# Optimization experiments

Hardware: AMD Instinct MI355X
Metric: run time of the kernel (lower is better)

Reference implementation:

```python
import jax, jax.numpy as jnp
import numpy as np

S, B, E, H, V, L = 128, 64, 512, 1024, 10000, 2


def setup_inputs() -> dict:
    key = jax.random.key(0)
    ks = jax.random.split(key, 10)
    s = 0.02  # weight scale ~ uniform(-k,k) magnitude
    return {
        "inputs": jax.random.randint(ks[0], (S, B), 0, V),
        "hidden": jnp.zeros((L, B, H), jnp.float32),
        "emb": jax.random.normal(ks[1], (V, E), jnp.float32) * 0.1,
        "Wx0": jax.random.normal(ks[2], (3, H, E), jnp.float32) * s,
        "Uh0": jax.random.normal(ks[3], (3, H, H), jnp.float32) * s,
        "b0": jax.random.normal(ks[4], (3, H), jnp.float32) * s,
        "Wx1": jax.random.normal(ks[5], (3, H, H), jnp.float32) * s,
        "Uh1": jax.random.normal(ks[6], (3, H, H), jnp.float32) * s,
        "b1": jax.random.normal(ks[7], (3, H), jnp.float32) * s,
        "Wd": jax.random.normal(ks[8], (V, H), jnp.float32) * 0.1,
        "bd": jnp.zeros((V,), jnp.float32),
    }


def _gru_cell(xp, h, U, b):
    # xp: (3,B,H) precomputed input projections in [r,z,h] order
    r = jax.nn.sigmoid(xp[0] + h @ U[0].T + b[0])
    z = jax.nn.sigmoid(xp[1] + h @ U[1].T + b[1])
    h_tilde = jnp.tanh(xp[2] + (r * h) @ U[2].T + b[2])
    return (1.0 - z) * h + z * h_tilde


def reference(inputs, hidden, emb, Wx0, Uh0, b0, Wx1, Uh1, b1, Wd, bd):
    x_embs = emb[inputs]                                   # [S,B,E]
    # precompute layer-0 input projections across all timesteps
    xa0 = jnp.einsum("sbe,goe->sgbo", x_embs, Wx0)        # [S,3,B,H]

    def step(carry, xa0_t):
        h0, h1 = carry
        h0n = _gru_cell(xa0_t, h0, Uh0, b0)
        xp1 = jnp.einsum("bk,gok->gbo", h0n, Wx1)          # [3,B,H]
        h1n = _gru_cell(xp1, h1, Uh1, b1)
        return (h0n, h1n), h1n

    (h0f, h1f), hs1 = jax.lax.scan(step, (hidden[0], hidden[1]), xa0)
    logits = jnp.einsum("sbh,vh->sbv", hs1, Wd) + bd       # [S,B,V]
    return logits, jnp.stack([h0f, h1f])
```

## Files before the change

kernel.cpp:

```cpp
#include <hip/hip_runtime.h>
#include <hip/hip_bf16.h>

#define SLEN 128
#define BAT 64
#define EDIM 512
#define HDIM 1024
#define VOC 10000
#define VPAD 10112
#define NWG_REC 192
#define TPB_REC 512

typedef short v8s __attribute__((ext_vector_type(8)));
typedef float v4f __attribute__((ext_vector_type(4)));
typedef unsigned short u16;

__device__ __forceinline__ u16 f2bf(float f) {
  unsigned u = __float_as_uint(f);
  u += 0x7fffu + ((u >> 16) & 1u);
  return (u16)(u >> 16);
}
__device__ __forceinline__ float bf2f(u16 b) {
  return __uint_as_float(((unsigned)b) << 16);
}
__device__ __forceinline__ float sigm(float x) { return 1.f / (1.f + __expf(-x)); }
__device__ __forceinline__ float tanh_f(float x) { return 1.f - 2.f / (1.f + __expf(2.f * x)); }

__device__ __forceinline__ void st_f32(float* p, float v) {
  __hip_atomic_store(p, v, __ATOMIC_RELAXED, __HIP_MEMORY_SCOPE_AGENT);
}
__device__ __forceinline__ float ld_f32(const float* p) {
  return __hip_atomic_load(p, __ATOMIC_RELAXED, __HIP_MEMORY_SCOPE_AGENT);
}
__device__ __forceinline__ float ld_bf16(const unsigned* base, int elem) {
  unsigned pr = __hip_atomic_load(base + (elem >> 1), __ATOMIC_RELAXED, __HIP_MEMORY_SCOPE_AGENT);
  return bf2f((u16)((elem & 1) ? (pr >> 16) : (pr & 0xffffu)));
}
__device__ __forceinline__ void st_bf16_pair(unsigned* base, int elem, u16 val, int l) {
  unsigned p = (unsigned)__shfl_xor((int)val, 1);
  if ((l & 1) == 0)
    __hip_atomic_store(base + (elem >> 1), (unsigned)val | (p << 16),
                       __ATOMIC_RELAXED, __HIP_MEMORY_SCOPE_AGENT);
}

__device__ __forceinline__ void gbar(int* bar, int ph, int wg, int t) {
  asm volatile("s_waitcnt vmcnt(0) lgkmcnt(0)" ::: "memory");
  __syncthreads();
  if (t == 0)
    __hip_atomic_store(&bar[wg], ph, __ATOMIC_RELAXED, __HIP_MEMORY_SCOPE_AGENT);
  if (t < 64) {
    for (;;) {
      int v0 = __hip_atomic_load(&bar[t],       __ATOMIC_RELAXED, __HIP_MEMORY_SCOPE_AGENT);
      int v1 = __hip_atomic_load(&bar[64 + t],  __ATOMIC_RELAXED, __HIP_MEMORY_SCOPE_AGENT);
      int v2 = __hip_atomic_load(&bar[128 + t], __ATOMIC_RELAXED, __HIP_MEMORY_SCOPE_AGENT);
      if (__all((v0 >= ph) & (v1 >= ph) & (v2 >= ph))) break;
      __builtin_amdgcn_s_sleep(1);
    }
  }
  __syncthreads();
}

__device__ __forceinline__ v4f gemm_staged(const char* Asrc, char* stage,
                                           const char* bb, int swz,
                                           int t, int rg, int lr, int lk2) {
  const char* gp = Asrc + (t >> 3) * 2048 + (t & 7) * 16;
  char* wp = stage + (t >> 3) * 128 + ((((t & 7) * 16)) ^ (((t >> 3) & 7) << 4));
  const char* rp = stage + (rg * 16 + lr) * 128;
  v4f acc{0.f, 0.f, 0.f, 0.f};
  v8s sreg[3];
  asm volatile("global_load_dwordx4 %0, %1, off sc0 sc1" : "=v"(sreg[0]) : "v"(gp));
  asm volatile("global_load_dwordx4 %0, %1, off offset:128 sc0 sc1" : "=v"(sreg[1]) : "v"(gp));
  asm volatile("global_load_dwordx4 %0, %1, off offset:256 sc0 sc1" : "=v"(sreg[2]) : "v"(gp));
  asm volatile("s_waitcnt vmcnt(2)" ::: "memory");
  __builtin_amdgcn_sched_barrier(0);
  *(v8s*)wp = sreg[0];
  __syncthreads();
#pragma unroll
  for (int c = 0; c < 16; ++c) {
    if (c < 13)
      asm volatile("global_load_dwordx4 %0, %1, off offset:%2 sc0 sc1"
                   : "=v"(sreg[c % 3]) : "v"(gp), "i"((c + 3) * 128));
    if (c < 15) {
      if (c < 13)       asm volatile("s_waitcnt vmcnt(2)" ::: "memory");
      else if (c == 13) asm volatile("s_waitcnt vmcnt(1)" ::: "memory");
      else              asm volatile("s_waitcnt vmcnt(0)" ::: "memory");
      __builtin_amdgcn_sched_barrier(0);
      *(v8s*)(wp + ((c + 1) & 1) * 8192) = sreg[(c + 1) % 3];
    }
    const char* buf = rp + (c & 1) * 8192;
#pragma unroll
    for (int ls = 0; ls < 2; ++ls) {
      v8s a = *(const v8s*)(buf + ((ls * 64 + lk2) ^ swz));
      v8s b = *(const v8s*)(bb + (((c * 2 + ls) * 64 + lk2) ^ swz));
      acc = __builtin_amdgcn_mfma_f32_16x16x32_bf16(a, b, acc, 0, 0, 0);
    }
    __syncthreads();
  }
  return acc;
}

__global__ void __launch_bounds__(TPB_REC, 2) k_recur(
    const u16* __restrict__ Uh0b, const u16* __restrict__ Wx1b, const u16* __restrict__ Uh1b,
    const float* __restrict__ b0, const float* __restrict__ b1,
    const u16* __restrict__ xa0,
    float* __restrict__ h0f, u16* __restrict__ h0b,
    float* __restrict__ h1f, u16* __restrict__ h1b,
    u16* __restrict__ a2, float* __restrict__ z0,
    u16* __restrict__ a5, float* __restrict__ z1,
    u16* __restrict__ xp1,
    u16* __restrict__ hs1,
    float* __restrict__ outh,
    int* __restrict__ bar) {
  extern __shared__ char smem[];
  const int wg = blockIdx.x;
  const int t = threadIdx.x;
  const int w = t >> 6;
  const int l = t & 63;
  const int lr = l & 15;
  const int lk2 = (l >> 4) * 16;
  const int rg = w >> 1, cg = w & 1;
  const int rbase = rg * 16 + ((l >> 4) << 2);
  const int swz = (lr & 7) << 4;
  char* stage = smem + 131072;

  unsigned* a2u  = (unsigned*)a2;
  unsigned* a5u  = (unsigned*)a5;
  unsigned* h0bu = (unsigned*)h0b;
  unsigned* h1bu = (unsigned*)h1b;
  unsigned* xpu  = (unsigned*)xp1;

  {
    const u16* w1src; int w1row0;
    if (wg < 64)       { w1src = Uh0b; w1row0 = wg * 32; }
    else if (wg < 160) { w1src = Wx1b; w1row0 = (wg - 64) * 32; }
    else               { w1src = Uh1b; w1row0 = 2048 + (wg - 160) * 32; }
    for (int i = t; i < 4096; i += TPB_REC) {
      int c = i >> 7, j = i & 127;
      v8s v = *(const v8s*)(w1src + (size_t)(w1row0 + c) * HDIM + j * 8);
      *(v8s*)(smem + c * 2048 + ((j * 16) ^ ((c & 7) << 4))) = v;
    }
    if (wg < 96) {
      const u16* w2src; int w2row0;
      if (wg < 32) { w2src = Uh0b; w2row0 = 2048 + wg * 32; }
      else         { w2src = Uh1b; w2row0 = (wg - 32) * 32; }
      for (int i = t; i < 4096; i += TPB_REC) {
        int c = i >> 7, j = i & 127;
        v8s v = *(const v8s*)(w2src + (size_t)(w2row0 + c) * HDIM + j * 8);
        *(v8s*)(smem + 65536 + c * 2048 + ((j * 16) ^ ((c & 7) << 4))) = v;
      }
    }
    __syncthreads();
  }

  const char* bb1 = smem + (cg * 16 + lr) * 2048;
  const char* bb2 = smem + 65536 + (cg * 16 + lr) * 2048;

  for (int T = 0; T <= SLEN + 1; ++T) {
    if (wg < 64) {
      if (T < SLEN) {
        const int cglob = wg * 32 + cg * 16 + lr;
        const int g = cglob >> 10;
        const int o = cglob & 1023;
        const float bias = b0[g * HDIM + o];
        float xv[4], hv[4];
#pragma unroll
        for (int r = 0; r < 4; ++r) {
          int b = rbase + r;
          xv[r] = bf2f(xa0[((T * 3 + g) * BAT + b) * HDIM + o]);
          if (g == 0) hv[r] = ld_f32(&h0f[b * HDIM + o]);
        }
        v4f acc = gemm_staged((const char*)h0b, stage, bb1, swz, t, rg, lr, lk2);
#pragma unroll
        for (int r = 0; r < 4; ++r) {
          int b = rbase + r;
          float s = sigm(acc[r] + xv[r] + bias);
          if (g == 0) st_bf16_pair(a2u, b * HDIM + o, f2bf(s * hv[r]), l);
          else        st_f32(&z0[b * HDIM + o], s);
        }
      }
    } else if (wg < 160) {
      if (T >= 1 && T <= SLEN) {
        const int n = (wg - 64) * 32 + cg * 16 + lr;
        v4f acc = gemm_staged((const char*)h0b, stage, bb1, swz, t, rg, lr, lk2);
        unsigned* xp = xpu + ((((T - 1) & 1) * (BAT * 3 * HDIM)) >> 1);
#pragma unroll
        for (int r = 0; r < 4; ++r)
          st_bf16_pair(xp, (rbase + r) * 3072 + n, f2bf(acc[r]), l);
      }
    } else {
      if (T >= 2) {
        const int t5 = T - 2;
        const int o = (wg - 160) * 32 + cg * 16 + lr;
        const unsigned* xp = xpu + (((t5 & 1) * (BAT * 3 * HDIM)) >> 1);
        const float bias = b1[2 * HDIM + o];
        float pv[4], zv[4], hv[4];
#pragma unroll
        for (int r = 0; r < 4; ++r) {
          int b = rbase + r;
          pv[r] = ld_bf16(xp, b * 3072 + 2048 + o);
          zv[r] = ld_f32(&z1[b * HDIM + o]);
          hv[r] = ld_f32(&h1f[b * HDIM + o]);
        }
        v4f acc = gemm_staged((const char*)a5, stage, bb1, swz, t, rg, lr, lk2);
#pragma unroll
        for (int r = 0; r < 4; ++r) {
          int b = rbase + r;
          float ht = tanh_f(pv[r] + acc[r] + bias);
          float hn = (1.f - zv[r]) * hv[r] + zv[r] * ht;
          u16 hb = f2bf(hn);
          st_f32(&h1f[b * HDIM + o], hn);
          st_bf16_pair(h1bu, b * HDIM + o, hb, l);
          hs1[((size_t)t5 * BAT + b) * HDIM + o] = hb;
          if (t5 == SLEN - 1) outh[(size_t)BAT * HDIM + b * HDIM + o] = hn;
        }
      }
    }
    gbar(bar, 2 * T + 1, wg, t);
    if (wg < 32) {
      if (T < SLEN) {
        const int o = wg * 32 + cg * 16 + lr;
        const float bias = b0[2 * HDIM + o];
        float xv[4], zv[4], hv[4];
#pragma unroll
        for (int r = 0; r < 4; ++r) {
          int b = rbase + r;
          xv[r] = bf2f(xa0[((T * 3 + 2) * BAT + b) * HDIM + o]);
          zv[r] = ld_f32(&z0[b * HDIM + o]);
          hv[r] = ld_f32(&h0f[b * HDIM + o]);
        }
        v4f acc = gemm_staged((const char*)a2, stage, bb2, swz, t, rg, lr, lk2);
#pragma unroll
        for (int r = 0; r < 4; ++r) {
          int b = rbase + r;
          float ht = tanh_f(xv[r] + acc[r] + bias);
          float hn = (1.f - zv[r]) * hv[r] + zv[r] * ht;
          st_f32(&h0f[b * HDIM + o], hn);
          st_bf16_pair(h0bu, b * HDIM + o, f2bf(hn), l);
          if (T == SLEN - 1) outh[b * HDIM + o] = hn;
        }
      }
    } else if (wg < 96) {
      if (T >= 1 && T <= SLEN) {
        const int t4 = T - 1;
        const int cglob = (wg - 32) * 32 + cg * 16 + lr;
        const int g = cglob >> 10;
        const int o = cglob & 1023;
        const unsigned* xp = xpu + (((t4 & 1) * (BAT * 3 * HDIM)) >> 1);
        const float bias = b1[g * HDIM + o];
        float pv[4], hv[4];
#pragma unroll
        for (int r = 0; r < 4; ++r) {
          int b = rbase + r;
          pv[r] = ld_bf16(xp, b * 3072 + g * HDIM + o);
          if (g == 0) hv[r] = ld_f32(&h1f[b * HDIM + o]);
        }
        v4f acc = gemm_staged((const char*)h1b, stage, bb2, swz, t, rg, lr, lk2);
#pragma unroll
        for (int r = 0; r < 4; ++r) {
          int b = rbase + r;
          float s = sigm(acc[r] + pv[r] + bias);
          if (g == 0) st_bf16_pair(a5u, b * HDIM + o, f2bf(s * hv[r]), l);
          else        st_f32(&z1[b * HDIM + o], s);
        }
      }
    }
    gbar(bar, 2 * T + 2, wg, t);
  }
}

template <int MODE>
__global__ void __launch_bounds__(256) k_gemm(
    const u16* __restrict__ A, const u16* __restrict__ Bw,
    const int* __restrict__ gidx, const float* __restrict__ bias,
    void* __restrict__ Out) {
  constexpr int K = MODE ? 1024 : 512;
  constexpr int NB_N = MODE ? (VPAD / 128) : (3072 / 128);

  __shared__ u16 sA[128 * 64];
  __shared__ u16 sB[128 * 64];

  const int nwg = gridDim.x;
  const int cpx = nwg >> 3;
  const int bid = blockIdx.x;
  const int swz = (bid & 7) * cpx + (bid >> 3);
  const int bm = swz / NB_N, bn = swz % NB_N;
  const int m0 = bm * 128, n0 = bn * 128;

  const int t = threadIdx.x;
  const int w = t >> 6, l = t & 63;
  const int lr = l & 15, lk = (l >> 4) * 8;
  const int wm = (w >> 1) * 64, wn = (w & 1) * 64;
  const int kc = (t & 7) * 8;

  int arowg[4];
#pragma unroll
  for (int i = 0; i < 4; ++i) {
    int row = m0 + i * 32 + (t >> 3);
    arowg[i] = (MODE == 0) ? gidx[row] : row;
  }
  int brow[4];
#pragma unroll
  for (int i = 0; i < 4; ++i) brow[i] = n0 + i * 32 + (t >> 3);

  v4f acc[4][4];
#pragma unroll
  for (int mi = 0; mi < 4; ++mi)
#pragma unroll
    for (int ni = 0; ni < 4; ++ni) acc[mi][ni] = v4f{0.f, 0.f, 0.f, 0.f};

  for (int k0 = 0; k0 < K; k0 += 64) {
    __syncthreads();
#pragma unroll
    for (int i = 0; i < 4; ++i) {
      const u16* src = A + (size_t)arowg[i] * K + k0 + kc;
      __builtin_amdgcn_global_load_lds((const __attribute__((address_space(1))) void*)src,
                                       (__attribute__((address_space(3))) void*)(sA + i * 2048 + w * 512),
                                       16, 0, 0);
    }
#pragma unroll
    for (int i = 0; i < 4; ++i) {
      const u16* src = Bw + (size_t)brow[i] * K + k0 + kc;
      __builtin_amdgcn_global_load_lds((const __attribute__((address_space(1))) void*)src,
                                       (__attribute__((address_space(3))) void*)(sB + i * 2048 + w * 512),
                                       16, 0, 0);
    }
    asm volatile("s_waitcnt vmcnt(0)" ::: "memory");
    __syncthreads();
#pragma unroll
    for (int ks = 0; ks < 2; ++ks) {
      v8s af[4], bfr[4];
#pragma unroll
      for (int mi = 0; mi < 4; ++mi) af[mi] = *(const v8s*)&sA[(wm + mi * 16 + lr) * 64 + ks * 32 + lk];
#pragma unroll
      for (int ni = 0; ni < 4; ++ni) bfr[ni] = *(const v8s*)&sB[(wn + ni * 16 + lr) * 64 + ks * 32 + lk];
#pragma unroll
      for (int mi = 0; mi < 4; ++mi)
#pragma unroll
        for (int ni = 0; ni < 4; ++ni)
          acc[mi][ni] = __builtin_amdgcn_mfma_f32_16x16x32_bf16(af[mi], bfr[ni], acc[mi][ni], 0, 0, 0);
    }
  }

#pragma unroll
  for (int mi = 0; mi < 4; ++mi)
#pragma unroll
    for (int ni = 0; ni < 4; ++ni)
#pragma unroll
      for (int r = 0; r < 4; ++r) {
        int grow = m0 + wm + mi * 16 + ((l >> 4) << 2) + r;
        int gcol = n0 + wn + ni * 16 + lr;
        float v = acc[mi][ni][r];
        if (MODE == 0) {
          int s = grow >> 6, b = grow & 63;
          int g = gcol >> 10, o = gcol & 1023;
          ((u16*)Out)[(((size_t)s * 3 + g) * BAT + b) * HDIM + o] = f2bf(v);
        } else {
          if (gcol < VOC) ((float*)Out)[(size_t)grow * VOC + gcol] = v + bias[gcol];
        }
      }
}

__global__ void k_cvt(const float* __restrict__ src, u16* __restrict__ dst, int n, int nsrc) {
  int i = (blockIdx.x * 256 + threadIdx.x) * 4;
  if (i >= n) return;
#pragma unroll
  for (int j = 0; j < 4; ++j) {
    int idx = i + j;
    if (idx < n) dst[idx] = (idx < nsrc) ? f2bf(src[idx]) : (u16)0;
  }
}

__global__ void k_init(const float* __restrict__ hidden,
                       float* h0f, u16* h0b, float* h1f, u16* h1b, int* bar) {
  int i = blockIdx.x * 256 + threadIdx.x;
  if (i < BAT * HDIM) {
    float v0 = hidden[i];
    float v1 = hidden[BAT * HDIM + i];
    h0f[i] = v0; h0b[i] = f2bf(v0);
    h1f[i] = v1; h1b[i] = f2bf(v1);
  }
  if (i < 512) bar[i] = 0;
}

extern "C" void kernel_launch(void* const* d_in, const int* in_sizes, int n_in,
                              void* d_out, int out_size, void* d_ws, size_t ws_size,
                              hipStream_t stream) {
  const int*   inp = (const int*)d_in[0];
  const float* hid = (const float*)d_in[1];
  const float* emb = (const float*)d_in[2];
  const float* Wx0 = (const float*)d_in[3];
  const float* Uh0 = (const float*)d_in[4];
  const float* b0  = (const float*)d_in[5];
  const float* Wx1 = (const float*)d_in[6];
  const float* Uh1 = (const float*)d_in[7];
  const float* b1  = (const float*)d_in[8];
  const float* Wd  = (const float*)d_in[9];
  const float* bd  = (const float*)d_in[10];

  char* ws = (char*)d_ws;
  size_t off = 0;
  auto alloc = [&](size_t bytes) {
    void* p = ws + off;
    off = (off + bytes + 255) & ~(size_t)255;
    return p;
  };
  u16* emb_b = (u16*)alloc(sizeof(u16) * (size_t)VOC * EDIM);
  u16* Wx0_b = (u16*)alloc(sizeof(u16) * 3 * HDIM * EDIM);
  u16* Uh0_b = (u16*)alloc(sizeof(u16) * 3 * HDIM * HDIM);
  u16* Wx1_b = (u16*)alloc(sizeof(u16) * 3 * HDIM * HDIM);
  u16* Uh1_b = (u16*)alloc(sizeof(u16) * 3 * HDIM * HDIM);
  u16* Wd_b  = (u16*)alloc(sizeof(u16) * (size_t)VPAD * HDIM);
  u16* xa0_b = (u16*)alloc(sizeof(u16) * (size_t)SLEN * 3 * BAT * HDIM);
  u16* hs1_b = (u16*)alloc(sizeof(u16) * (size_t)SLEN * BAT * HDIM);
  u16* xp1   = (u16*)alloc(sizeof(u16) * 2 * BAT * 3 * HDIM);
  float* h0f = (float*)alloc(sizeof(float) * BAT * HDIM);
  float* h1f = (float*)alloc(sizeof(float) * BAT * HDIM);
  u16* h0b   = (u16*)alloc(sizeof(u16) * BAT * HDIM);
  u16* h1b   = (u16*)alloc(sizeof(u16) * BAT * HDIM);
  u16* a2    = (u16*)alloc(sizeof(u16) * BAT * HDIM);
  u16* a5    = (u16*)alloc(sizeof(u16) * BAT * HDIM);
  float* z0  = (float*)alloc(sizeof(float) * BAT * HDIM);
  float* z1  = (float*)alloc(sizeof(float) * BAT * HDIM);
  int* bar   = (int*)alloc(sizeof(int) * 512);

  float* logits = (float*)d_out;
  float* outh = logits + (size_t)SLEN * BAT * VOC;

  auto cvt = [&](const float* s, u16* d, int n, int nsrc) {
    k_cvt<<<dim3((n / 4 + 255) / 256), dim3(256), 0, stream>>>(s, d, n, nsrc);
  };
  cvt(emb, emb_b, VOC * EDIM, VOC * EDIM);
  cvt(Wx0, Wx0_b, 3 * HDIM * EDIM, 3 * HDIM * EDIM);
  cvt(Uh0, Uh0_b, 3 * HDIM * HDIM, 3 * HDIM * HDIM);
  cvt(Wx1, Wx1_b, 3 * HDIM * HDIM, 3 * HDIM * HDIM);
  cvt(Uh1, Uh1_b, 3 * HDIM * HDIM, 3 * HDIM * HDIM);
  cvt(Wd, Wd_b, VPAD * HDIM, VOC * HDIM);
  k_init<<<dim3(256), dim3(256), 0, stream>>>(hid, h0f, h0b, h1f, h1b, bar);

  k_gemm<0><<<dim3(64 * 24), dim3(256), 0, stream>>>(emb_b, Wx0_b, inp, (const float*)nullptr, (void*)xa0_b);

  (void)hipFuncSetAttribute(reinterpret_cast<const void*>(k_recur),
                            hipFuncAttributeMaxDynamicSharedMemorySize, 147456);
  k_recur<<<dim3(NWG_REC), dim3(TPB_REC), 147456, stream>>>(
      Uh0_b, Wx1_b, Uh1_b, b0, b1, xa0_b,
      h0f, h0b, h1f, h1b, a2, z0, a5, z1, xp1, hs1_b, outh, bar);

  k_gemm<1><<<dim3(64 * 79), dim3(256), 0, stream>>>(hs1_b, Wd_b, (const int*)nullptr, bd, d_out);
}
```

Baseline: 2.730 ms.

## Replace global grid barriers with per-group dataflow flags and double-buffered state

Replaces the two all-workgroup barriers per timestep in the persistent GRU recurrence with per-workgroup progress flags, so each role polls only the producers it depends on. Hidden state, gate and projection buffers are double-buffered by timestep parity so producers can run ahead without write-after-read hazards. Workgroups are remapped to 256 with dedicated roles for the r/z gates, candidate states of both layers, and the layer-1 input projection. This targets barrier latency on the sequential critical path. The cost is more workspace, finer-grained polling traffic, and more complex ordering that has to be correct.

```diff
diff --git a/kernel.cpp b/kernel.cpp
--- a/kernel.cpp
+++ b/kernel.cpp
@@ -7,7 +7,7 @@
 #define HDIM 1024
 #define VOC 10000
 #define VPAD 10112
-#define NWG_REC 192
+#define NWG_REC 256
 #define TPB_REC 512
 
 typedef short v8s __attribute__((ext_vector_type(8)));
@@ -42,28 +42,11 @@
                        __ATOMIC_RELAXED, __HIP_MEMORY_SCOPE_AGENT);
 }
 
-__device__ __forceinline__ void gbar(int* bar, int ph, int wg, int t) {
-  asm volatile("s_waitcnt vmcnt(0) lgkmcnt(0)" ::: "memory");
-  __syncthreads();
-  if (t == 0)
-    __hip_atomic_store(&bar[wg], ph, __ATOMIC_RELAXED, __HIP_MEMORY_SCOPE_AGENT);
-  if (t < 64) {
-    for (;;) {
-      int v0 = __hip_atomic_load(&bar[t],       __ATOMIC_RELAXED, __HIP_MEMORY_SCOPE_AGENT);
-      int v1 = __hip_atomic_load(&bar[64 + t],  __ATOMIC_RELAXED, __HIP_MEMORY_SCOPE_AGENT);
-      int v2 = __hip_atomic_load(&bar[128 + t], __ATOMIC_RELAXED, __HIP_MEMORY_SCOPE_AGENT);
-      if (__all((v0 >= ph) & (v1 >= ph) & (v2 >= ph))) break;
-      __builtin_amdgcn_s_sleep(1);
-    }
-  }
-  __syncthreads();
-}
-
 __device__ __forceinline__ v4f gemm_staged(const char* Asrc, char* stage,
                                            const char* bb, int swz,
                                            int t, int rg, int lr, int lk2) {
   const char* gp = Asrc + (t >> 3) * 2048 + (t & 7) * 16;
-  char* wp = stage + (t >> 3) * 128 + ((((t & 7) * 16)) ^ (((t >> 3) & 7) << 4));
+  char* wp = stage + (t >> 3) * 128 + (((t & 7) * 16) ^ (((t >> 3) & 7) << 4));
   const char* rp = stage + (rg * 16 + lr) * 128;
   v4f acc{0.f, 0.f, 0.f, 0.f};
   v8s sreg[3];
@@ -97,6 +80,27 @@
   }
   return acc;
 }
+
+#define POLL(COND)                                   \
+  do {                                               \
+    if (t < 64) {                                    \
+      for (;;) {                                     \
+        bool ok_ = (COND);                           \
+        if (__all(ok_)) break;                       \
+        __builtin_amdgcn_s_sleep(1);                 \
+      }                                              \
+    }                                                \
+    __syncthreads();                                 \
+  } while (0)
+
+#define FENCE_FLAG(FIDX)                                                        \
+  do {                                                                          \
+    asm volatile("s_waitcnt vmcnt(0) lgkmcnt(0)" ::: "memory");                 \
+    __syncthreads();                                                            \
+    if (t == 0)                                                                 \
+      __hip_atomic_store(&bar[FIDX], T + 1, __ATOMIC_RELAXED,                   \
+                         __HIP_MEMORY_SCOPE_AGENT);                             \
+  } while (0)
 
 __global__ void __launch_bounds__(TPB_REC, 2) k_recur(
     const u16* __restrict__ Uh0b, const u16* __restrict__ Wx1b, const u16* __restrict__ Uh1b,
@@ -128,23 +132,26 @@
   unsigned* h1bu = (unsigned*)h1b;
   unsigned* xpu  = (unsigned*)xp1;
 
+  auto lf = [&](int i) {
+    return __hip_atomic_load(&bar[i], __ATOMIC_RELAXED, __HIP_MEMORY_SCOPE_AGENT);
+  };
+
   {
     const u16* w1src; int w1row0;
     if (wg < 64)       { w1src = Uh0b; w1row0 = wg * 32; }
-    else if (wg < 160) { w1src = Wx1b; w1row0 = (wg - 64) * 32; }
-    else               { w1src = Uh1b; w1row0 = 2048 + (wg - 160) * 32; }
+    else if (wg < 96)  { w1src = Uh0b; w1row0 = 2048 + (wg - 64) * 32; }
+    else if (wg < 192) { w1src = Wx1b; w1row0 = (wg - 96) * 32; }
+    else               { w1src = Uh1b; w1row0 = (wg - 192) * 32; }
     for (int i = t; i < 4096; i += TPB_REC) {
       int c = i >> 7, j = i & 127;
       v8s v = *(const v8s*)(w1src + (size_t)(w1row0 + c) * HDIM + j * 8);
       *(v8s*)(smem + c * 2048 + ((j * 16) ^ ((c & 7) << 4))) = v;
     }
-    if (wg < 96) {
-      const u16* w2src; int w2row0;
-      if (wg < 32) { w2src = Uh0b; w2row0 = 2048 + wg * 32; }
-      else         { w2src = Uh1b; w2row0 = (wg - 32) * 32; }
+    if (wg >= 64 && wg < 96) {
+      int w2row0 = 2048 + (wg - 64) * 32;
       for (int i = t; i < 4096; i += TPB_REC) {
         int c = i >> 7, j = i & 127;
-        v8s v = *(const v8s*)(w2src + (size_t)(w2row0 + c) * HDIM + j * 8);
+        v8s v = *(const v8s*)(Uh1b + (size_t)(w2row0 + c) * HDIM + j * 8);
         *(v8s*)(smem + 65536 + c * 2048 + ((j * 16) ^ ((c & 7) << 4))) = v;
       }
     }
@@ -154,116 +161,133 @@
   const char* bb1 = smem + (cg * 16 + lr) * 2048;
   const char* bb2 = smem + 65536 + (cg * 16 + lr) * 2048;
 
-  for (int T = 0; T <= SLEN + 1; ++T) {
-    if (wg < 64) {
+  if (wg < 64) {
+    const int g = wg >> 5;
+    const int o = (wg * 32 + cg * 16 + lr) & 1023;
+    const float bias = b0[g * HDIM + o];
+    for (int T = 0; T <= SLEN + 1; ++T) {
       if (T < SLEN) {
-        const int cglob = wg * 32 + cg * 16 + lr;
-        const int g = cglob >> 10;
-        const int o = cglob & 1023;
-        const float bias = b0[g * HDIM + o];
+        if (T >= 1) POLL(lf(64 + (t & 31)) >= T);
+        const int pr = (T - 1) & 1, pw = T & 1;
         float xv[4], hv[4];
 #pragma unroll
         for (int r = 0; r < 4; ++r) {
           int b = rbase + r;
           xv[r] = bf2f(xa0[((T * 3 + g) * BAT + b) * HDIM + o]);
-          if (g == 0) hv[r] = ld_f32(&h0f[b * HDIM + o]);
-        }
-        v4f acc = gemm_staged((const char*)h0b, stage, bb1, swz, t, rg, lr, lk2);
+          if (g == 0) hv[r] = ld_f32(h0f + pr * 65536 + b * HDIM + o);
+        }
+        v4f acc = gemm_staged((const char*)(h0b + pr * 65536), stage, bb1, swz, t, rg, lr, lk2);
 #pragma unroll
         for (int r = 0; r < 4; ++r) {
           int b = rbase + r;
           float s = sigm(acc[r] + xv[r] + bias);
-          if (g == 0) st_bf16_pair(a2u, b * HDIM + o, f2bf(s * hv[r]), l);
-          else        st_f32(&z0[b * HDIM + o], s);
-        }
-      }
-    } else if (wg < 160) {
+          if (g == 0) st_bf16_pair(a2u + pw * 32768, b * HDIM + o, f2bf(s * hv[r]), l);
+          else        st_f32(z0 + pw * 65536 + b * HDIM + o, s);
+        }
+      }
+      FENCE_FLAG(wg);
+    }
+  } else if (wg < 96) {
+    const int j = wg - 64;
+    const int o = j * 32 + cg * 16 + lr;
+    const float bias0 = b0[2 * HDIM + o];
+    const float bias1 = b1[2 * HDIM + o];
+    for (int T = 0; T <= SLEN + 1; ++T) {
+      if (T < SLEN) {
+        POLL(lf(t & 31) >= T + 1);
+        const int pr = (T - 1) & 1, pw = T & 1;
+        float xv[4], hv[4];
+#pragma unroll
+        for (int r = 0; r < 4; ++r) {
+          int b = rbase + r;
+          xv[r] = bf2f(xa0[((T * 3 + 2) * BAT + b) * HDIM + o]);
+          hv[r] = ld_f32(h0f + pr * 65536 + b * HDIM + o);
+        }
+        v4f acc = gemm_staged((const char*)(a2 + pw * 65536), stage, bb1, swz, t, rg, lr, lk2);
+        POLL(lf(32 + (t & 31)) >= T + 1 && lf(128 + t) >= T && lf(192 + (t & 31)) >= T);
+        float zv[4];
+#pragma unroll
+        for (int r = 0; r < 4; ++r) zv[r] = ld_f32(z0 + pw * 65536 + (rbase + r) * HDIM + o);
+#pragma unroll
+        for (int r = 0; r < 4; ++r) {
+          int b = rbase + r;
+          float ht = tanh_f(xv[r] + acc[r] + bias0);
+          float hn = (1.f - zv[r]) * hv[r] + zv[r] * ht;
+          st_f32(h0f + pw * 65536 + b * HDIM + o, hn);
+          st_bf16_pair(h0bu + pw * 32768, b * HDIM + o, f2bf(hn), l);
+          if (T == SLEN - 1) outh[b * HDIM + o] = hn;
+        }
+      }
+      FENCE_FLAG(64 + j);
+      if (T >= 2) {
+        const int t5 = T - 2, p5 = t5 & 1, pm = (T - 3) & 1;
+        POLL(lf(224 + t) >= T + 1);
+        v4f acc = gemm_staged((const char*)(a5 + p5 * 65536), stage, bb2, swz, t, rg, lr, lk2);
+        float pv[4], zv[4], hv[4];
+#pragma unroll
+        for (int r = 0; r < 4; ++r) {
+          int b = rbase + r;
+          pv[r] = ld_bf16(xpu + p5 * 98304, b * 3072 + 2048 + o);
+          zv[r] = ld_f32(z1 + p5 * 65536 + b * HDIM + o);
+          hv[r] = ld_f32(h1f + pm * 65536 + b * HDIM + o);
+        }
+#pragma unroll
+        for (int r = 0; r < 4; ++r) {
+          int b = rbase + r;
+          float ht = tanh_f(pv[r] + acc[r] + bias1);
+          float hn = (1.f - zv[r]) * hv[r] + zv[r] * ht;
+          u16 hb = f2bf(hn);
+          st_f32(h1f + p5 * 65536 + b * HDIM + o, hn);
+          st_bf16_pair(h1bu + p5 * 32768, b * HDIM + o, hb, l);
+          hs1[((size_t)t5 * BAT + b) * HDIM + o] = hb;
+          if (t5 == SLEN - 1) outh[(size_t)BAT * HDIM + b * HDIM + o] = hn;
+        }
+      }
+      FENCE_FLAG(96 + j);
+    }
+  } else if (wg < 192) {
+    const int j = wg - 96;
+    const int n = j * 32 + cg * 16 + lr;
+    for (int T = 0; T <= SLEN + 1; ++T) {
       if (T >= 1 && T <= SLEN) {
-        const int n = (wg - 64) * 32 + cg * 16 + lr;
-        v4f acc = gemm_staged((const char*)h0b, stage, bb1, swz, t, rg, lr, lk2);
-        unsigned* xp = xpu + ((((T - 1) & 1) * (BAT * 3 * HDIM)) >> 1);
+        POLL(lf(64 + (t & 31)) >= T && lf(96 + (t & 31)) >= T);
+        const int ts = T - 1, ps = ts & 1;
+        v4f acc = gemm_staged((const char*)(h0b + ps * 65536), stage, bb1, swz, t, rg, lr, lk2);
+        unsigned* xp = xpu + ps * 98304;
 #pragma unroll
         for (int r = 0; r < 4; ++r)
           st_bf16_pair(xp, (rbase + r) * 3072 + n, f2bf(acc[r]), l);
       }
-    } else {
+      FENCE_FLAG(128 + j);
+    }
+  } else {
+    const int j = wg - 192;
+    const int g = j >> 5;
+    const int o = (j * 32 + cg * 16 + lr) & 1023;
+    const float bias = b1[g * HDIM + o];
+    for (int T = 0; T <= SLEN + 1; ++T) {
       if (T >= 2) {
-        const int t5 = T - 2;
-        const int o = (wg - 160) * 32 + cg * 16 + lr;
-        const unsigned* xp = xpu + (((t5 & 1) * (BAT * 3 * HDIM)) >> 1);
-        const float bias = b1[2 * HDIM + o];
-        float pv[4], zv[4], hv[4];
-#pragma unroll
-        for (int r = 0; r < 4; ++r) {
-          int b = rbase + r;
-          pv[r] = ld_bf16(xp, b * 3072 + 2048 + o);
-          zv[r] = ld_f32(&z1[b * HDIM + o]);
-          hv[r] = ld_f32(&h1f[b * HDIM + o]);
-        }
-        v4f acc = gemm_staged((const char*)a5, stage, bb1, swz, t, rg, lr, lk2);
-#pragma unroll
-        for (int r = 0; r < 4; ++r) {
-          int b = rbase + r;
-          float ht = tanh_f(pv[r] + acc[r] + bias);
-          float hn = (1.f - zv[r]) * hv[r] + zv[r] * ht;
-          u16 hb = f2bf(hn);
-          st_f32(&h1f[b * HDIM + o], hn);
-          st_bf16_pair(h1bu, b * HDIM + o, hb, l);
-          hs1[((size_t)t5 * BAT + b) * HDIM + o] = hb;
-          if (t5 == SLEN - 1) outh[(size_t)BAT * HDIM + b * HDIM + o] = hn;
-        }
-      }
-    }
-    gbar(bar, 2 * T + 1, wg, t);
-    if (wg < 32) {
-      if (T < SLEN) {
-        const int o = wg * 32 + cg * 16 + lr;
-        const float bias = b0[2 * HDIM + o];
-        float xv[4], zv[4], hv[4];
-#pragma unroll
-        for (int r = 0; r < 4; ++r) {
-          int b = rbase + r;
-          xv[r] = bf2f(xa0[((T * 3 + 2) * BAT + b) * HDIM + o]);
-          zv[r] = ld_f32(&z0[b * HDIM + o]);
-          hv[r] = ld_f32(&h0f[b * HDIM + o]);
-        }
-        v4f acc = gemm_staged((const char*)a2, stage, bb2, swz, t, rg, lr, lk2);
-#pragma unroll
-        for (int r = 0; r < 4; ++r) {
-          int b = rbase + r;
-          float ht = tanh_f(xv[r] + acc[r] + bias);
-          float hn = (1.f - zv[r]) * hv[r] + zv[r] * ht;
-          st_f32(&h0f[b * HDIM + o], hn);
-          st_bf16_pair(h0bu, b * HDIM + o, f2bf(hn), l);
-          if (T == SLEN - 1) outh[b * HDIM + o] = hn;
-        }
-      }
-    } else if (wg < 96) {
-      if (T >= 1 && T <= SLEN) {
-        const int t4 = T - 1;
-        const int cglob = (wg - 32) * 32 + cg * 16 + lr;
-        const int g = cglob >> 10;
-        const int o = cglob & 1023;
-        const unsigned* xp = xpu + (((t4 & 1) * (BAT * 3 * HDIM)) >> 1);
-        const float bias = b1[g * HDIM + o];
+        POLL(lf(96 + (t & 31)) >= T);
+        const int ts = T - 2, ps = ts & 1, pm = (T - 3) & 1;
+        v4f acc = gemm_staged((const char*)(h1b + pm * 65536), stage, bb1, swz, t, rg, lr, lk2);
+        POLL(lf(128 + t) >= T && lf(192 + (t & 31)) >= T);
         float pv[4], hv[4];
 #pragma unroll
         for (int r = 0; r < 4; ++r) {
           int b = rbase + r;
-          pv[r] = ld_bf16(xp, b * 3072 + g * HDIM + o);
-          if (g == 0) hv[r] = ld_f32(&h1f[b * HDIM + o]);
-        }
-        v4f acc = gemm_staged((const char*)h1b, stage, bb2, swz, t, rg, lr, lk2);
+          pv[r] = ld_bf16(xpu + ps * 98304, b * 3072 + g * HDIM + o);
+          if (g == 0) hv[r] = ld_f32(h1f + pm * 65536 + b * HDIM + o);
+        }
 #pragma unroll
         for (int r = 0; r < 4; ++r) {
           int b = rbase + r;
           float s = sigm(acc[r] + pv[r] + bias);
-          if (g == 0) st_bf16_pair(a5u, b * HDIM + o, f2bf(s * hv[r]), l);
-          else        st_f32(&z1[b * HDIM + o], s);
-        }
-      }
-    }
-    gbar(bar, 2 * T + 2, wg, t);
+          if (g == 0) st_bf16_pair(a5u + ps * 32768, b * HDIM + o, f2bf(s * hv[r]), l);
+          else        st_f32(z1 + ps * 65536 + b * HDIM + o, s);
+        }
+      }
+      FENCE_FLAG(224 + j);
+    }
   }
 }
 
@@ -375,8 +399,8 @@
   if (i < BAT * HDIM) {
     float v0 = hidden[i];
     float v1 = hidden[BAT * HDIM + i];
-    h0f[i] = v0; h0b[i] = f2bf(v0);
-    h1f[i] = v1; h1b[i] = f2bf(v1);
+    h0f[65536 + i] = v0; h0b[65536 + i] = f2bf(v0);
+    h1f[65536 + i] = v1; h1b[65536 + i] = f2bf(v1);
   }
   if (i < 512) bar[i] = 0;
 }
@@ -412,14 +436,14 @@
   u16* xa0_b = (u16*)alloc(sizeof(u16) * (size_t)SLEN * 3 * BAT * HDIM);
   u16* hs1_b = (u16*)alloc(sizeof(u16) * (size_t)SLEN * BAT * HDIM);
   u16* xp1   = (u16*)alloc(sizeof(u16) * 2 * BAT * 3 * HDIM);
-  float* h0f = (float*)alloc(sizeof(float) * BAT * HDIM);
-  float* h1f = (float*)alloc(sizeof(float) * BAT * HDIM);
-  u16* h0b   = (u16*)alloc(sizeof(u16) * BAT * HDIM);
-  u16* h1b   = (u16*)alloc(sizeof(u16) * BAT * HDIM);
-  u16* a2    = (u16*)alloc(sizeof(u16) * BAT * HDIM);
-  u16* a5    = (u16*)alloc(sizeof(u16) * BAT * HDIM);
-  float* z0  = (float*)alloc(sizeof(float) * BAT * HDIM);
-  float* z1  = (float*)alloc(sizeof(float) * BAT * HDIM);
+  float* h0f = (float*)alloc(sizeof(float) * 2 * BAT * HDIM);
+  float* h1f = (float*)alloc(sizeof(float) * 2 * BAT * HDIM);
+  u16* h0b   = (u16*)alloc(sizeof(u16) * 2 * BAT * HDIM);
+  u16* h1b   = (u16*)alloc(sizeof(u16) * 2 * BAT * HDIM);
+  u16* a2    = (u16*)alloc(sizeof(u16) * 2 * BAT * HDIM);
+  u16* a5    = (u16*)alloc(sizeof(u16) * 2 * BAT * HDIM);
+  float* z0  = (float*)alloc(sizeof(float) * 2 * BAT * HDIM);
+  float* z1  = (float*)alloc(sizeof(float) * 2 * BAT * HDIM);
   int* bar   = (int*)alloc(sizeof(int) * 512);
 
   float* logits = (float*)d_out;
```

After: 2.880 ms. 1.06x slower.
